# Kernel optimization log

Measured on AMD Instinct MI355X. Metric: run time of the kernel, lower is better.

Reference implementation:

```python
import jax, jax.numpy as jnp
from jax import lax
import numpy as np

# dims: T turns per dialogue, B dialogues, H = inpt_size (utter hidden), UE user embed,
# PE position embed, S = conv feature size, DEG avg in-degree
T, B, H, UE, PE, DEG = 30, 512, 256, 10, 16, 8
S = H + UE + PE          # 282, GRUCell(size, size)
OUT = 256                # context_hidden_size (output_size of linear2)
N = B * T                # merged graph nodes
E = N * DEG              # merged graph edges
LN_EPS = 1e-5


def _gru_cell(x, h, wih, whh, bih, bhh):
    # torch nn.GRUCell gate order: r, z, n
    gx = x @ wih.T + bih
    gh = h @ whh.T + bhh
    xr, xz, xn = jnp.split(gx, 3, axis=-1)
    hr, hz, hn = jnp.split(gh, 3, axis=-1)
    r = jax.nn.sigmoid(xr + hr)
    z = jax.nn.sigmoid(xz + hz)
    n = jnp.tanh(xn + r * hn)
    return (1.0 - z) * n + z * h


def _run_gru(xs, wih, whh, bih, bhh, reverse):
    # xs: [T, B, Din]; torch nn.GRU with zero initial hidden
    h0 = jnp.zeros((xs.shape[1], whh.shape[1]), xs.dtype)
    def step(h, x):
        hn = _gru_cell(x, h, wih, whh, bih, bhh)
        return hn, hn
    hT, ys = lax.scan(step, h0, xs, reverse=reverse)
    return ys, hT


def _forward(utter_hidden, ub, edge_weight,
             wih_f, whh_f, bih_f, bhh_f, wih_b, whh_b, bih_b, bhh_b,
             lin1_w, lin1_b, posemb,
             c1_wih, c1_whh, c1_bih, c1_bhh,
             c2_wih, c2_whh, c2_bih, c2_bhh,
             g1_w, g1_b, g2_w, g2_b, g3_w, g3_b,
             ln_g, ln_b, lin2_w, lin2_b, edge_index):
    # --- bidirectional GRU over turns + linear1 (GatedGCNContext.rnn) ---
    inp = jnp.concatenate([utter_hidden, ub], axis=-1)        # [T, B, H+UE]
    ys_f, h_f = _run_gru(inp, wih_f, whh_f, bih_f, bhh_f, False)
    ys_b, h_b = _run_gru(inp, wih_b, whh_b, bih_b, bhh_b, True)
    rnn_x = jnp.tanh(jnp.concatenate([ys_f, ys_b], -1) @ lin1_w.T + lin1_b)  # [T,B,H]
    # --- merged graph node features (PyG batching is batch-major) ---
    x0 = rnn_x.transpose(1, 0, 2).reshape(N, H)               # node b*T+t
    pos = posemb[jnp.tile(jnp.arange(T), B)]                  # [N, PE]
    ub_flat = ub.reshape(-1, UE)                              # faithful to original (turn-major)
    cell1 = (c1_wih, c1_whh, c1_bih, c1_bhh)
    cell2 = (c2_wih, c2_whh, c2_bih, c2_bhh)
    src, dst = edge_index[0], edge_index[1]

    def conv(xin, gw, gb):
        # message: edge_weight * GRUCell1(x_j, x_i); aggregate: scatter-add; update: Linear(GRUCell2(aggr, x))
        m = edge_weight[:, None] * _gru_cell(xin[src], xin[dst], *cell1)   # [E, S]
        aggr = jax.ops.segment_sum(m, dst, num_segments=N)                 # [N, S]
        return _gru_cell(aggr, xin, *cell2) @ gw.T + gb                    # [N, H]

    x1 = jnp.tanh(conv(jnp.concatenate([x0, pos, ub_flat], 1), g1_w, g1_b))
    x2 = jnp.tanh(conv(jnp.concatenate([x1, pos, ub_flat], 1), g2_w, g2_b))
    x3 = jnp.tanh(conv(jnp.concatenate([x2, pos, ub_flat], 1), g3_w, g3_b))
    xs = jnp.tanh(x1 + x2 + x3)
    mu = xs.mean(-1, keepdims=True)
    var = ((xs - mu) ** 2).mean(-1, keepdims=True)
    xs = ln_g * (xs - mu) / jnp.sqrt(var + LN_EPS) + ln_b     # LayerNorm (dropout = eval identity)
    gx = xs.reshape(B, T, H).transpose(1, 0, 2)               # chunk+stack+permute -> [T, B, H]
    out = jnp.tanh(jnp.concatenate([rnn_x, gx], -1) @ lin2_w.T + lin2_b)   # [T, B, OUT]
    return out


def setup_inputs() -> dict:
    key = jax.random.key(0)
    ks = iter(jax.random.split(key, 40))
    def p(shape):
        return jax.random.normal(next(ks), shape, dtype=jnp.float32) * 0.05
    # block-diagonal batched graph: per dialogue b, each node t receives DEG random in-edges
    rng = np.random.default_rng(0)
    off = (np.arange(B) * T)[:, None, None]
    src = rng.integers(0, T, size=(B, T, DEG)) + off
    dst = np.broadcast_to(np.arange(T)[None, :, None], (B, T, DEG)) + off
    edge_index = jnp.asarray(np.stack([src.ravel(), dst.ravel()]), dtype=jnp.int32)
    return {
        "utter_hidden": jax.random.normal(next(ks), (T, B, H), jnp.float32),
        "ub": jax.random.normal(next(ks), (T, B, UE), jnp.float32),
        "edge_weight": jax.random.uniform(next(ks), (E,), jnp.float32),
        "wih_f": p((3 * H, H + UE)), "whh_f": p((3 * H, H)), "bih_f": jnp.zeros((3 * H,)), "bhh_f": jnp.zeros((3 * H,)),
        "wih_b": p((3 * H, H + UE)), "whh_b": p((3 * H, H)), "bih_b": jnp.zeros((3 * H,)), "bhh_b": jnp.zeros((3 * H,)),
        "lin1_w": p((H, 2 * H)), "lin1_b": jnp.zeros((H,)),
        "posemb": p((100, PE)),
        "c1_wih": p((3 * S, S)), "c1_whh": p((3 * S, S)), "c1_bih": jnp.zeros((3 * S,)), "c1_bhh": jnp.zeros((3 * S,)),
        "c2_wih": p((3 * S, S)), "c2_whh": p((3 * S, S)), "c2_bih": jnp.zeros((3 * S,)), "c2_bhh": jnp.zeros((3 * S,)),
        "g1_w": p((H, S)), "g1_b": jnp.zeros((H,)),
        "g2_w": p((H, S)), "g2_b": jnp.zeros((H,)),
        "g3_w": p((H, S)), "g3_b": jnp.zeros((H,)),
        "ln_g": jnp.ones((H,)), "ln_b": jnp.zeros((H,)),
        "lin2_w": p((OUT, 2 * H)), "lin2_b": jnp.zeros((OUT,)),
        "edge_index": edge_index,
    }


def reference(utter_hidden, ub, edge_weight,
              wih_f, whh_f, bih_f, bhh_f, wih_b, whh_b, bih_b, bhh_b,
              lin1_w, lin1_b, posemb,
              c1_wih, c1_whh, c1_bih, c1_bhh,
              c2_wih, c2_whh, c2_bih, c2_bhh,
              g1_w, g1_b, g2_w, g2_b, g3_w, g3_b,
              ln_g, ln_b, lin2_w, lin2_b, edge_index):
    return _forward(utter_hidden, ub, edge_weight,
                    wih_f, whh_f, bih_f, bhh_f, wih_b, whh_b, bih_b, bhh_b,
                    lin1_w, lin1_b, posemb,
                    c1_wih, c1_whh, c1_bih, c1_bhh,
                    c2_wih, c2_whh, c2_bih, c2_bhh,
                    g1_w, g1_b, g2_w, g2_b, g3_w, g3_b,
                    ln_g, ln_b, lin2_w, lin2_b, edge_index)
```

## Files before the change

### kernel.cpp

```cpp
#include <hip/hip_runtime.h>
#include <math.h>

#define T_DIM 30
#define B_DIM 512
#define S_DIM 282
#define NB (T_DIM*B_DIM)
#define E_DIM (NB*8)
#define G3 846
#define GST 2538
#define KXP 288

typedef __attribute__((ext_vector_type(8))) short bf16x8;
typedef __attribute__((ext_vector_type(4))) float f32x4;

__device__ __forceinline__ float sigm(float x){ return 1.f/(1.f+expf(-x)); }

__device__ __forceinline__ ushort f2b(float f){
  union { float f; unsigned u; } v; v.f = f;
  unsigned r = v.u + 0x7fffu + ((v.u >> 16) & 1u);
  return (ushort)(r >> 16);
}
__device__ __forceinline__ float b2f(ushort b){
  union { unsigned u; float f; } v; v.u = ((unsigned)b) << 16; return v.f;
}
__device__ __forceinline__ void f2b2(float v, ushort& hi, ushort& lo){
  hi = f2b(v);
  lo = f2b(v - b2f(hi));
}

#define GLDS16(g, l) __builtin_amdgcn_global_load_lds( \
    (const __attribute__((address_space(1))) void*)(g), \
    (__attribute__((address_space(3))) void*)(l), 16, 0, 0)

__global__ __launch_bounds__(256, 2) void mfma_gemm3(
    const ushort* __restrict__ A, const ushort* __restrict__ W,
    const float* __restrict__ bias, float* __restrict__ C,
    int Nreal, int Kp, int ldc, int act, ushort* __restrict__ xout)
{
  __shared__ char smem[65536];

  int gx = gridDim.x;
  int h = blockIdx.y*gx + blockIdx.x;
  int nwg = gx*gridDim.y;
  int bx, by;
  if ((nwg & 7) == 0) {
    int q = nwg >> 3;
    int lwg = (h & 7)*q + (h >> 3);
    by = lwg / gx; bx = lwg - by*gx;
  } else { by = blockIdx.y; bx = blockIdx.x; }

  int tid  = threadIdx.x;
  int w    = tid >> 6;
  int lane = tid & 63;
  int lr = lane & 15;
  int lk = lane >> 4;
  int row0 = by*128;
  int col0 = bx*128;
  size_t astr = 2*(size_t)Kp;
  int NK = Kp >> 5;

  auto stage = [&](int buf, int kt){
    int kk = kt*32;
    char* Ab = smem + buf*32768;
    char* Wb = Ab + 16384;
    #pragma unroll
    for (int i = 0; i < 4; ++i) {
      int sb = w*256 + i*64;
      int s  = sb + lane;
      int r  = s >> 3;
      int rl = (s & 7) ^ (r & 7);
      int p  = rl >> 2, ks = rl & 3;
      const ushort* ga = A + (size_t)(row0 + r)*astr + (size_t)p*Kp + kk + ks*8;
      GLDS16(ga, Ab + sb*16);
      const ushort* gw = W + (size_t)(col0 + r)*astr + (size_t)p*Kp + kk + ks*8;
      GLDS16(gw, Wb + sb*16);
    }
  };
  auto rdfrag = [&](char* base, int r, int p)->bf16x8{
    int byte = r*128 + (((p*64) + lk*16) ^ ((r & 7) << 4));
    return *reinterpret_cast<const bf16x8*>(base + byte);
  };

  f32x4 acc[2][8] = {};
  stage(0, 0);
  __syncthreads();

  for (int kt = 0; kt < NK; ++kt) {
    int cur = kt & 1;
    if (kt + 1 < NK) stage(cur ^ 1, kt + 1);
    char* Ab = smem + cur*32768;
    char* Wb = Ab + 16384;

    bf16x8 a[2][2], b[8][2];
    #pragma unroll
    for (int i = 0; i < 2; ++i)
      #pragma unroll
      for (int p = 0; p < 2; ++p)
        a[i][p] = rdfrag(Ab, w*32 + i*16 + lr, p);
    #pragma unroll
    for (int j = 0; j < 8; ++j)
      #pragma unroll
      for (int p = 0; p < 2; ++p)
        b[j][p] = rdfrag(Wb, j*16 + lr, p);

    #pragma unroll
    for (int j = 0; j < 8; ++j) {
      acc[0][j] = __builtin_amdgcn_mfma_f32_16x16x32_bf16(a[0][0], b[j][0], acc[0][j], 0,0,0);
      acc[0][j] = __builtin_amdgcn_mfma_f32_16x16x32_bf16(a[0][1], b[j][0], acc[0][j], 0,0,0);
      acc[0][j] = __builtin_amdgcn_mfma_f32_16x16x32_bf16(a[0][0], b[j][1], acc[0][j], 0,0,0);
      acc[1][j] = __builtin_amdgcn_mfma_f32_16x16x32_bf16(a[1][0], b[j][0], acc[1][j], 0,0,0);
      acc[1][j] = __builtin_amdgcn_mfma_f32_16x16x32_bf16(a[1][1], b[j][0], acc[1][j], 0,0,0);
      acc[1][j] = __builtin_amdgcn_mfma_f32_16x16x32_bf16(a[1][0], b[j][1], acc[1][j], 0,0,0);
    }
    __syncthreads();
  }

  #pragma unroll
  for (int i = 0; i < 2; ++i) {
    #pragma unroll
    for (int j = 0; j < 8; ++j) {
      int cc = col0 + j*16 + lr;
      if (cc >= Nreal) continue;
      float bv = bias[cc];
      #pragma unroll
      for (int r = 0; r < 4; ++r) {
        int rr = row0 + w*32 + i*16 + lk*4 + r;
        float v = acc[i][j][r] + bv;
        if (act) v = tanhf(v);
        C[(size_t)rr*ldc + cc] = v;
        if (xout && cc < 256) {
          ushort hi, lo; f2b2(v, hi, lo);
          xout[(size_t)rr*2*KXP + cc]       = hi;
          xout[(size_t)rr*2*KXP + KXP + cc] = lo;
        }
      }
    }
  }
}

static inline void mgemm3(const ushort* A, const ushort* W, const float* bias,
                          float* C, int Nreal, int Npad, int Kp, int ldc,
                          int act, ushort* xout, hipStream_t s)
{
  dim3 grid((Npad + 127)/128, NB/128);
  mfma_gemm3<<<grid, 256, 0, s>>>(A, W, bias, C, Nreal, Kp, ldc, act, xout);
}

__global__ void cast_w(const float* __restrict__ w, ushort* __restrict__ wb,
                       int Nreal, int K, int Kp, int Npad)
{
  int idx = blockIdx.x*256 + threadIdx.x;
  if (idx >= Npad*Kp) return;
  int n = idx / Kp, k = idx - n*Kp;
  float v = (n < Nreal && k < K) ? w[(size_t)n*K + k] : 0.f;
  ushort hi, lo; f2b2(v, hi, lo);
  wb[(size_t)n*2*Kp + k]      = hi;
  wb[(size_t)n*2*Kp + Kp + k] = lo;
}
static inline void castw(const float* w, ushort* wb, int Nreal, int K, int Kp,
                         int Npad, hipStream_t s)
{
  int tot = Npad*Kp;
  cast_w<<<(tot+255)/256, 256, 0, s>>>(w, wb, Nreal, K, Kp, Npad);
}

__global__ void copy_f(const float* __restrict__ s, float* __restrict__ d, int n)
{
  int i = blockIdx.x*256 + threadIdx.x;
  if (i < n) d[i] = s[i];
}

__global__ void transpose_whh(const float* __restrict__ w, float* __restrict__ wt)
{
  int idx = blockIdx.x*256 + threadIdx.x;
  if (idx < 768*256) { int r = idx >> 8, c = idx & 255; wt[c*768 + r] = w[idx]; }
}

__global__ void build_inp(const float* __restrict__ utter, const float* __restrict__ ub,
                          ushort* __restrict__ inp)
{
  int r = blockIdx.x;
  for (int c = threadIdx.x; c < KXP; c += 128){
    float v = 0.f;
    if (c < 256)      v = utter[(size_t)r*256 + c];
    else if (c < 266) v = ub[(size_t)r*10 + (c-256)];
    ushort hi, lo; f2b2(v, hi, lo);
    inp[(size_t)r*2*KXP + c]       = hi;
    inp[(size_t)r*2*KXP + KXP + c] = lo;
  }
}

__global__ __launch_bounds__(256) void gru_step(
    const float* __restrict__ gx,
    const float* __restrict__ wtf, const float* __restrict__ bhh_f,
    const float* __restrict__ wtb, const float* __restrict__ bhh_b,
    float* __restrict__ ys_f, float* __restrict__ ys_b, int t)
{
  int dir = blockIdx.z;
  const float* wt  = dir ? wtb  : wtf;
  const float* bhh = dir ? bhh_b : bhh_f;
  float* ys = dir ? ys_b : ys_f;
  int tt = dir ? (T_DIM-1 - t) : t;
  const float* hprev = nullptr;
  if (t > 0) hprev = ys + (size_t)(dir ? tt+1 : tt-1) * B_DIM * 256;

  int tx = threadIdx.x & 63;
  int ty = threadIdx.x >> 6;
  int j = blockIdx.x * 64 + tx;
  int b = blockIdx.y * 4 + ty;

  __shared__ float sh[4][256];
  for (int i = threadIdx.x; i < 4*256; i += 256) {
    int bb = i >> 8, kk = i & 255;
    int gb = blockIdx.y*4 + bb;
    sh[bb][kk] = hprev ? hprev[(size_t)gb*256 + kk] : 0.f;
  }
  __syncthreads();

  float ar = bhh[j], az = bhh[256+j], an = bhh[512+j];
  for (int k = 0; k < 256; ++k) {
    float h = sh[ty][k];
    const float* wk = wt + (size_t)k*768;
    ar += h * wk[j];
    az += h * wk[256+j];
    an += h * wk[512+j];
  }
  size_t base = ((size_t)tt*B_DIM + b)*1536 + (size_t)dir*768;
  float r = sigm(gx[base + j]       + ar);
  float z = sigm(gx[base + 256 + j] + az);
  float n = tanhf(gx[base + 512 + j] + r*an);
  float h = sh[ty][j];
  ys[((size_t)tt*B_DIM + b)*256 + j] = (1.f - z)*n + z*h;
}

__global__ void build_cat(const float* __restrict__ a, const float* __restrict__ b2,
                          ushort* __restrict__ c, int mapmode)
{
  int r = blockIdx.x;
  int r2 = r;
  if (mapmode){ int t = r >> 9, bb = r & 511; r2 = bb*T_DIM + t; }
  for (int cix = threadIdx.x; cix < 512; cix += 128){
    float v = (cix < 256) ? a[(size_t)r*256 + cix] : b2[(size_t)r2*256 + (cix-256)];
    ushort hi, lo; f2b2(v, hi, lo);
    c[(size_t)r*1024 + cix]       = hi;
    c[(size_t)r*1024 + 512 + cix] = lo;
  }
}

__global__ void build_xin(const float* __restrict__ xsrc, int reorder,
                          const float* __restrict__ posemb, const float* __restrict__ ub,
                          ushort* __restrict__ xin)
{
  int n = blockIdx.x;
  int b = n / T_DIM, t = n % T_DIM;
  int srow = reorder ? (t*B_DIM + b) : n;
  for (int s = threadIdx.x; s < KXP; s += 128){
    float v = 0.f;
    if (s < 256)      v = xsrc[(size_t)srow*256 + s];
    else if (s < 272) v = posemb[t*16 + (s-256)];
    else if (s < 282) v = ub[(size_t)n*10 + (s-272)];
    ushort hi, lo; f2b2(v, hi, lo);
    xin[(size_t)n*2*KXP + s]       = hi;
    xin[(size_t)n*2*KXP + KXP + s] = lo;
  }
}

__global__ __launch_bounds__(128) void edge_aggr(
    const float* __restrict__ gate, const ushort* __restrict__ xin,
    const int* __restrict__ esrc, const int* __restrict__ edst,
    const float* __restrict__ ew, ushort* __restrict__ aggr)
{
  int e0 = blockIdx.x * 8;
  __shared__ int ssrc[8]; __shared__ float sw[8]; __shared__ int sdst;
  if (threadIdx.x < 8) { ssrc[threadIdx.x] = esrc[e0+threadIdx.x]; sw[threadIdx.x] = ew[e0+threadIdx.x]; }
  if (threadIdx.x == 0) sdst = edst[e0];
  __syncthreads();
  int i = sdst;
  for (int s = threadIdx.x; s < KXP; s += 128) {
    if (s >= S_DIM) {
      aggr[(size_t)i*2*KXP + s] = 0; aggr[(size_t)i*2*KXP + KXP + s] = 0; continue;
    }
    size_t gi = (size_t)i*GST;
    float hr = gate[gi + 846 + s];
    float hz = gate[gi + 1128 + s];
    float hn = gate[gi + 1410 + s];
    float hv = b2f(xin[(size_t)i*2*KXP + s]) + b2f(xin[(size_t)i*2*KXP + KXP + s]);
    float acc = 0.f;
    #pragma unroll
    for (int d = 0; d < 8; ++d) {
      size_t gj = (size_t)ssrc[d]*GST; float w = sw[d];
      float xr = gate[gj + s];
      float xz = gate[gj + 282 + s];
      float xn = gate[gj + 564 + s];
      float r = sigm(xr + hr);
      float z = sigm(xz + hz);
      float n = tanhf(xn + r*hn);
      acc += w * ((1.f - z)*n + z*hv);
    }
    ushort hi, lo; f2b2(acc, hi, lo);
    aggr[(size_t)i*2*KXP + s]       = hi;
    aggr[(size_t)i*2*KXP + KXP + s] = lo;
  }
}

__global__ __launch_bounds__(128) void gru2_combine(
    const float* __restrict__ gate, const ushort* __restrict__ xin,
    ushort* __restrict__ upd)
{
  int n = blockIdx.x;
  for (int s = threadIdx.x; s < KXP; s += 128) {
    if (s >= S_DIM) {
      upd[(size_t)n*2*KXP + s] = 0; upd[(size_t)n*2*KXP + KXP + s] = 0; continue;
    }
    size_t g = (size_t)n*GST;
    float xr = gate[g + 846 + s];
    float xz = gate[g + 1128 + s];
    float xn = gate[g + 1410 + s];
    float hr = gate[g + 1692 + s];
    float hz = gate[g + 1974 + s];
    float hn = gate[g + 2256 + s];
    float h  = b2f(xin[(size_t)n*2*KXP + s]) + b2f(xin[(size_t)n*2*KXP + KXP + s]);
    float r = sigm(xr + hr);
    float z = sigm(xz + hz);
    float nn = tanhf(xn + r*hn);
    ushort hi, lo; f2b2((1.f - z)*nn + z*h, hi, lo);
    upd[(size_t)n*2*KXP + s]       = hi;
    upd[(size_t)n*2*KXP + KXP + s] = lo;
  }
}

__global__ __launch_bounds__(256) void sum_ln(
    const float* __restrict__ x1, const float* __restrict__ x2, const float* __restrict__ x3,
    const float* __restrict__ g, const float* __restrict__ bta, float* __restrict__ out)
{
  int n = blockIdx.x; int j = threadIdx.x;
  size_t idx = (size_t)n*256 + j;
  float v = tanhf(x1[idx] + x2[idx] + x3[idx]);
  float s = v, sq = v*v;
  #pragma unroll
  for (int o = 32; o; o >>= 1) { s += __shfl_down(s, o, 64); sq += __shfl_down(sq, o, 64); }
  __shared__ float wsm[4], ws2[4];
  int lane = j & 63, w = j >> 6;
  if (lane == 0){ wsm[w] = s; ws2[w] = sq; }
  __syncthreads();
  float mean = (wsm[0]+wsm[1]+wsm[2]+wsm[3]) * (1.f/256.f);
  float m2   = (ws2[0]+ws2[1]+ws2[2]+ws2[3]) * (1.f/256.f);
  float var = m2 - mean*mean;
  float inv = rsqrtf(var + 1e-5f);
  out[idx] = g[j]*(v-mean)*inv + bta[j];
}

extern "C" void kernel_launch(void* const* d_in, const int* in_sizes, int n_in,
                              void* d_out, int out_size, void* d_ws, size_t ws_size,
                              hipStream_t stream)
{
  const float* utter = (const float*)d_in[0];
  const float* ub    = (const float*)d_in[1];
  const float* ew    = (const float*)d_in[2];
  const float* wih_f = (const float*)d_in[3];
  const float* whh_f = (const float*)d_in[4];
  const float* bih_f = (const float*)d_in[5];
  const float* bhh_f = (const float*)d_in[6];
  const float* wih_b = (const float*)d_in[7];
  const float* whh_b = (const float*)d_in[8];
  const float* bih_b = (const float*)d_in[9];
  const float* bhh_b = (const float*)d_in[10];
  const float* lin1_w= (const float*)d_in[11];
  const float* lin1_b= (const float*)d_in[12];
  const float* posemb= (const float*)d_in[13];
  const float* c1_wih= (const float*)d_in[14];
  const float* c1_whh= (const float*)d_in[15];
  const float* c1_bih= (const float*)d_in[16];
  const float* c1_bhh= (const float*)d_in[17];
  const float* c2_wih= (const float*)d_in[18];
  const float* c2_whh= (const float*)d_in[19];
  const float* c2_bih= (const float*)d_in[20];
  const float* c2_bhh= (const float*)d_in[21];
  const float* gw[3] = {(const float*)d_in[22], (const float*)d_in[24], (const float*)d_in[26]};
  const float* gb[3] = {(const float*)d_in[23], (const float*)d_in[25], (const float*)d_in[27]};
  const float* ln_g  = (const float*)d_in[28];
  const float* ln_b  = (const float*)d_in[29];
  const float* lin2_w= (const float*)d_in[30];
  const float* lin2_b= (const float*)d_in[31];
  const int*   eidx  = (const int*)d_in[32];
  const int* esrc = eidx;
  const int* edst = eidx + E_DIM;
  (void)ws_size; (void)n_in; (void)in_sizes; (void)out_size;

  float* ws = (float*)d_ws;
  size_t o = 0;
  auto A  = [&](size_t n){ size_t r = o; o += (n+3)&~(size_t)3; return r; };
  auto AU = [&](size_t n){ return A((n+1)/2); };

  size_t bGATE = A((size_t)NB*GST);
  size_t bYF   = A((size_t)NB*256);
  size_t bYB   = A((size_t)NB*256);
  size_t bRNN  = A((size_t)NB*256);
  size_t bBT   = A(2560);
  size_t bBX   = A(1536);
  size_t bB2   = A(896);
  size_t uXIN = AU((size_t)NB*2*KXP);
  size_t uAGG = AU((size_t)NB*2*KXP);
  size_t uWC1 = AU((size_t)2560*2*KXP);
  size_t uWXP = AU((size_t)1536*2*KXP);
  size_t uW2X = AU((size_t)896*2*KXP);
  size_t uG0  = AU((size_t)256*2*KXP);
  size_t uG1  = AU((size_t)256*2*KXP);
  size_t uG2  = AU((size_t)256*2*KXP);
  size_t uL1  = AU((size_t)256*2*512);
  size_t uL2  = AU((size_t)256*2*512);

  ushort* us = (ushort*)d_ws;
  auto U = [&](size_t fo){ return us + fo*2; };
  float* gate = ws + bGATE;
  float* wtf = gate + 23592960;
  float* wtb = wtf + 196608;
  ushort* uINP  = (ushort*)(ws + bYF);
  ushort* uCAT  = (ushort*)gate;
  float*  x3    = gate;

  castw(wih_f,  U(uWXP),                       768, 266,  KXP, 768, stream);
  castw(wih_b,  U(uWXP) + (size_t)768*2*KXP,   768, 266,  KXP, 768, stream);
  castw(c1_wih, U(uWC1),                       846, S_DIM, KXP, 846, stream);
  castw(c1_whh, U(uWC1) + (size_t)846*2*KXP,   846, S_DIM, KXP, 846, stream);
  castw(c2_whh, U(uWC1) + (size_t)1692*2*KXP,  846, S_DIM, KXP, 868, stream);
  castw(c2_wih, U(uW2X),                       846, S_DIM, KXP, 896, stream);
  castw(gw[0],  U(uG0), 256, S_DIM, KXP, 256, stream);
  castw(gw[1],  U(uG1), 256, S_DIM, KXP, 256, stream);
  castw(gw[2],  U(uG2), 256, S_DIM, KXP, 256, stream);
  castw(lin1_w, U(uL1), 256, 512, 512, 256, stream);
  castw(lin2_w, U(uL2), 256, 512, 512, 256, stream);
  const ushort* uGW[3] = {U(uG0), U(uG1), U(uG2)};
  copy_f<<<(846+255)/256,256,0,stream>>>(c1_bih, ws+bBT,        846);
  copy_f<<<(846+255)/256,256,0,stream>>>(c1_bhh, ws+bBT+846,    846);
  copy_f<<<(846+255)/256,256,0,stream>>>(c2_bhh, ws+bBT+1692,   846);
  copy_f<<<(768+255)/256,256,0,stream>>>(bih_f,  ws+bBX,        768);
  copy_f<<<(768+255)/256,256,0,stream>>>(bih_b,  ws+bBX+768,    768);
  copy_f<<<(846+255)/256,256,0,stream>>>(c2_bih, ws+bB2,        846);

  transpose_whh<<<(768*256+255)/256, 256, 0, stream>>>(whh_f, wtf);
  transpose_whh<<<(768*256+255)/256, 256, 0, stream>>>(whh_b, wtb);
  build_inp<<<NB, 128, 0, stream>>>(utter, ub, uINP);
  mgemm3(uINP, U(uWXP), ws+bBX, gate, 1536, 1536, KXP, 1536, 0, nullptr, stream);
  for (int t = 0; t < T_DIM; ++t)
    gru_step<<<dim3(4,128,2), 256, 0, stream>>>(gate, wtf, bhh_f, wtb, bhh_b,
                                                ws+bYF, ws+bYB, t);
  build_cat<<<NB, 128, 0, stream>>>(ws+bYF, ws+bYB, uCAT, 0);
  mgemm3(uCAT, U(uL1), lin1_b, ws+bRNN, 256, 256, 512, 256, 1, nullptr, stream);

  build_xin<<<NB, 128, 0, stream>>>(ws+bRNN, 1, posemb, ub, U(uXIN));
  float* XL[3] = {ws+bYF, ws+bYB, x3};
  for (int l = 0; l < 3; ++l) {
    mgemm3(U(uXIN), U(uWC1), ws+bBT, gate, 2538, 2560, KXP, GST, 0, nullptr, stream);
    edge_aggr<<<NB, 128, 0, stream>>>(gate, U(uXIN), esrc, edst, ew, U(uAGG));
    mgemm3(U(uAGG), U(uW2X), ws+bB2, gate + 846, 846, 896, KXP, GST, 0, nullptr, stream);
    gru2_combine<<<NB, 128, 0, stream>>>(gate, U(uXIN), U(uAGG));
    mgemm3(U(uAGG), uGW[l], gb[l], XL[l], 256, 256, KXP, 256, 1,
           (l < 2) ? U(uXIN) : nullptr, stream);
  }

  sum_ln<<<NB, 256, 0, stream>>>(XL[0], XL[1], XL[2], ln_g, ln_b, ws+bYF);
  build_cat<<<NB, 128, 0, stream>>>(ws+bRNN, ws+bYF, uCAT, 1);
  mgemm3(uCAT, U(uL2), lin2_b, (float*)d_out, 256, 256, 512, 256, 1, nullptr, stream);
}
```

Measured before the change: 1.923 ms.

## Compute two batch rows per GRU-step thread, fuse bias copies, remap edge-aggregation blocks

The recurrent GRU step kernel now handles 8 batch rows per block, with each thread computing two rows. Each Whh weight load is reused twice, halving weight traffic per step at the cost of fewer blocks and more registers. The six bias-copy launches are merged into one kernel. The edge_aggr block-to-node mapping is permuted so that concurrently running blocks touch nodes spread across the graph, possibly changing cache and channel behaviour.

```diff
diff --git a/kernel.cpp b/kernel.cpp
--- a/kernel.cpp
+++ b/kernel.cpp
@@ -164,10 +164,17 @@
   cast_w<<<(tot+255)/256, 256, 0, s>>>(w, wb, Nreal, K, Kp, Npad);
 }
 
-__global__ void copy_f(const float* __restrict__ s, float* __restrict__ d, int n)
+__global__ void copy_bias(const float* __restrict__ c1_bih, const float* __restrict__ c1_bhh,
+                          const float* __restrict__ c2_bhh, const float* __restrict__ bih_f,
+                          const float* __restrict__ bih_b, const float* __restrict__ c2_bih,
+                          float* __restrict__ bt, float* __restrict__ bx, float* __restrict__ b2)
 {
   int i = blockIdx.x*256 + threadIdx.x;
-  if (i < n) d[i] = s[i];
+  if (i < 846) {
+    bt[i] = c1_bih[i]; bt[846+i] = c1_bhh[i]; bt[1692+i] = c2_bhh[i];
+    b2[i] = c2_bih[i];
+  }
+  if (i < 768) { bx[i] = bih_f[i]; bx[768+i] = bih_b[i]; }
 }
 
 __global__ void transpose_whh(const float* __restrict__ w, float* __restrict__ wt)
@@ -201,36 +208,43 @@
   const float* bhh = dir ? bhh_b : bhh_f;
   float* ys = dir ? ys_b : ys_f;
   int tt = dir ? (T_DIM-1 - t) : t;
-  const float* hprev = nullptr;
-  if (t > 0) hprev = ys + (size_t)(dir ? tt+1 : tt-1) * B_DIM * 256;
+  const float* hprev = (t > 0) ? ys + (size_t)(dir ? tt+1 : tt-1)*B_DIM*256 : nullptr;
 
   int tx = threadIdx.x & 63;
   int ty = threadIdx.x >> 6;
   int j = blockIdx.x * 64 + tx;
-  int b = blockIdx.y * 4 + ty;
-
-  __shared__ float sh[4][256];
-  for (int i = threadIdx.x; i < 4*256; i += 256) {
+  int b0 = blockIdx.y * 8 + ty*2;
+
+  __shared__ float sh[8][256];
+  for (int i = threadIdx.x; i < 8*256; i += 256) {
     int bb = i >> 8, kk = i & 255;
-    int gb = blockIdx.y*4 + bb;
+    int gb = blockIdx.y*8 + bb;
     sh[bb][kk] = hprev ? hprev[(size_t)gb*256 + kk] : 0.f;
   }
   __syncthreads();
 
-  float ar = bhh[j], az = bhh[256+j], an = bhh[512+j];
+  float ar0 = bhh[j], az0 = bhh[256+j], an0 = bhh[512+j];
+  float ar1 = ar0, az1 = az0, an1 = an0;
+  const float* h0p = sh[ty*2];
+  const float* h1p = sh[ty*2+1];
   for (int k = 0; k < 256; ++k) {
-    float h = sh[ty][k];
     const float* wk = wt + (size_t)k*768;
-    ar += h * wk[j];
-    az += h * wk[256+j];
-    an += h * wk[512+j];
-  }
-  size_t base = ((size_t)tt*B_DIM + b)*1536 + (size_t)dir*768;
-  float r = sigm(gx[base + j]       + ar);
-  float z = sigm(gx[base + 256 + j] + az);
-  float n = tanhf(gx[base + 512 + j] + r*an);
-  float h = sh[ty][j];
-  ys[((size_t)tt*B_DIM + b)*256 + j] = (1.f - z)*n + z*h;
+    float wr = wk[j], wz = wk[256+j], wn = wk[512+j];
+    float h0 = h0p[k], h1 = h1p[k];
+    ar0 += h0*wr; az0 += h0*wz; an0 += h0*wn;
+    ar1 += h1*wr; az1 += h1*wz; an1 += h1*wn;
+  }
+  #pragma unroll
+  for (int bb = 0; bb < 2; ++bb) {
+    int b = b0 + bb;
+    size_t base = ((size_t)tt*B_DIM + b)*1536 + (size_t)dir*768;
+    float ar = bb ? ar1 : ar0, az = bb ? az1 : az0, an = bb ? an1 : an0;
+    float r = sigm(gx[base + j]       + ar);
+    float z = sigm(gx[base + 256 + j] + az);
+    float n = tanhf(gx[base + 512 + j] + r*an);
+    float h = sh[ty*2+bb][j];
+    ys[((size_t)tt*B_DIM + b)*256 + j] = (1.f - z)*n + z*h;
+  }
 }
 
 __global__ void build_cat(const float* __restrict__ a, const float* __restrict__ b2,
@@ -270,7 +284,9 @@
     const int* __restrict__ esrc, const int* __restrict__ edst,
     const float* __restrict__ ew, ushort* __restrict__ aggr)
 {
-  int e0 = blockIdx.x * 8;
+  int bid = blockIdx.x;
+  int node = (bid & 7)*(NB/8) + (bid >> 3);
+  int e0 = node * 8;
   __shared__ int ssrc[8]; __shared__ float sw[8]; __shared__ int sdst;
   if (threadIdx.x < 8) { ssrc[threadIdx.x] = esrc[e0+threadIdx.x]; sw[threadIdx.x] = ew[e0+threadIdx.x]; }
   if (threadIdx.x == 0) sdst = edst[e0];
@@ -431,20 +447,16 @@
   castw(lin1_w, U(uL1), 256, 512, 512, 256, stream);
   castw(lin2_w, U(uL2), 256, 512, 512, 256, stream);
   const ushort* uGW[3] = {U(uG0), U(uG1), U(uG2)};
-  copy_f<<<(846+255)/256,256,0,stream>>>(c1_bih, ws+bBT,        846);
-  copy_f<<<(846+255)/256,256,0,stream>>>(c1_bhh, ws+bBT+846,    846);
-  copy_f<<<(846+255)/256,256,0,stream>>>(c2_bhh, ws+bBT+1692,   846);
-  copy_f<<<(768+255)/256,256,0,stream>>>(bih_f,  ws+bBX,        768);
-  copy_f<<<(768+255)/256,256,0,stream>>>(bih_b,  ws+bBX+768,    768);
-  copy_f<<<(846+255)/256,256,0,stream>>>(c2_bih, ws+bB2,        846);
+  copy_bias<<<4, 256, 0, stream>>>(c1_bih, c1_bhh, c2_bhh, bih_f, bih_b, c2_bih,
+                                   ws+bBT, ws+bBX, ws+bB2);
 
   transpose_whh<<<(768*256+255)/256, 256, 0, stream>>>(whh_f, wtf);
   transpose_whh<<<(768*256+255)/256, 256, 0, stream>>>(whh_b, wtb);
   build_inp<<<NB, 128, 0, stream>>>(utter, ub, uINP);
   mgemm3(uINP, U(uWXP), ws+bBX, gate, 1536, 1536, KXP, 1536, 0, nullptr, stream);
   for (int t = 0; t < T_DIM; ++t)
-    gru_step<<<dim3(4,128,2), 256, 0, stream>>>(gate, wtf, bhh_f, wtb, bhh_b,
-                                                ws+bYF, ws+bYB, t);
+    gru_step<<<dim3(4,64,2), 256, 0, stream>>>(gate, wtf, bhh_f, wtb, bhh_b,
+                                               ws+bYF, ws+bYB, t);
   build_cat<<<NB, 128, 0, stream>>>(ws+bYF, ws+bYB, uCAT, 0);
   mgemm3(uCAT, U(uL1), lin1_b, ws+bRNN, 256, 256, 512, 256, 1, nullptr, stream);
 
```

After: 1.826 ms. 5.0% less time.
